# Performance work log

Measured on AMD Instinct MI355X. Metric: run time of the kernel, lower is better.

## Reference

```python
import jax, jax.numpy as jnp
import numpy as np

B, N, IN_DIM, ATT_DIM = 2, 8192, 512, 512


def setup_inputs() -> dict:
    key = jax.random.key(0)
    k1, k2, k3, k4 = jax.random.split(key, 4)
    X = jax.random.normal(k1, (B, N, IN_DIM), dtype=jnp.float32)
    adj = jax.random.uniform(k2, (B, N, N), dtype=jnp.float32)
    mask = jnp.ones((B, N), dtype=jnp.float32)
    # Learned params (torch Linear stores W as (out,in); we store (in,out) for x @ W)
    Wqk = jax.random.normal(k3, (IN_DIM, 2 * ATT_DIM), dtype=jnp.float32) / np.sqrt(IN_DIM)
    Wv = jax.random.normal(k4, (IN_DIM, IN_DIM), dtype=jnp.float32) / np.sqrt(IN_DIM)
    return {"X": X, "adj": adj, "mask": mask, "Wqk": Wqk, "Wv": Wv}


def reference(X, adj, mask, Wqk, Wv):
    # q, k: (B, N, att_dim); v: (B, N, in_dim)
    qk = X @ Wqk
    q, k = jnp.split(qk, 2, axis=-1)
    v = X @ Wv
    att_dim = q.shape[-1]
    inv_scale = 1.0 / jnp.sqrt(jnp.float32(att_dim))
    # Original math: w_i = inv_scale * sum_j adj_ij * m_i * m_j * (q_i . k_j).
    # Since the rank-1 mask factors (m_i m_j), fold m_j into k and m_i into the row
    # score, avoiding a second materialized NxN tensor:
    k_m = k * mask[:, :, None]                       # (B, N, att_dim)
    agg = jnp.einsum("bij,bjd->bid", adj, k_m)       # (B, N, att_dim)
    w = inv_scale * mask * jnp.einsum("bid,bid->bi", q, agg)  # (B, N)
    # softmax over the bag dimension (dim=1), then scale v rows
    L = jax.nn.softmax(w, axis=1)[:, :, None] * v    # (B, N, in_dim)
    return L
```

## Files before the change

kernel.cpp:

```cpp
#include <hip/hip_runtime.h>
#include <math.h>

#define BB 2
#define NN 8192
#define DD 512

static const float INV_SCALE = 0.04419417382415922f;

typedef short s16x8 __attribute__((ext_vector_type(8)));
typedef unsigned short u16x8 __attribute__((ext_vector_type(8)));
typedef float f32x4 __attribute__((ext_vector_type(4)));

#define AS1 __attribute__((address_space(1)))
#define AS3 __attribute__((address_space(3)))

__device__ __forceinline__ unsigned short bfbits(__bf16 h) {
    return __builtin_bit_cast(unsigned short, h);
}

__device__ __forceinline__ void gll16(const void* g, void* l) {
    __builtin_amdgcn_global_load_lds((const AS1 unsigned int*)g, (AS3 unsigned int*)l, 16, 0, 0);
}

__global__ __launch_bounds__(256) void convx_k(
    const float* __restrict__ X, unsigned short* __restrict__ Xhi,
    unsigned short* __restrict__ Xlo)
{
    long i = (long)blockIdx.x * 256 + threadIdx.x;
    float4 x = ((const float4*)X)[i];
    __bf16 h0 = (__bf16)x.x, h1 = (__bf16)x.y, h2 = (__bf16)x.z, h3 = (__bf16)x.w;
    ushort4 hi4 = make_ushort4(bfbits(h0), bfbits(h1), bfbits(h2), bfbits(h3));
    __bf16 l0 = (__bf16)(x.x - (float)h0), l1 = (__bf16)(x.y - (float)h1);
    __bf16 l2 = (__bf16)(x.z - (float)h2), l3 = (__bf16)(x.w - (float)h3);
    ushort4 lo4 = make_ushort4(bfbits(l0), bfbits(l1), bfbits(l2), bfbits(l3));
    ((ushort4*)Xhi)[i] = hi4;
    ((ushort4*)Xlo)[i] = lo4;
}

__global__ __launch_bounds__(256) void convw_k(
    const float* __restrict__ Wqk, const float* __restrict__ Wv,
    unsigned short* __restrict__ QTh, unsigned short* __restrict__ QTl,
    unsigned short* __restrict__ VTh, unsigned short* __restrict__ VTl)
{
    int i = blockIdx.x * 256 + threadIdx.x;
    float val; unsigned short *ph, *pl;
    if (i < 524288) {
        int n = i >> 9, k = i & 511;
        val = Wqk[k * 1024 + n]; ph = QTh + i; pl = QTl + i;
    } else {
        int o = i - 524288; int n = o >> 9, k = o & 511;
        val = Wv[k * 512 + n]; ph = VTh + o; pl = VTl + o;
    }
    __bf16 h = (__bf16)val;
    __bf16 l = (__bf16)(val - (float)h);
    *ph = bfbits(h); *pl = bfbits(l);
}

template <int EPI, int NT, bool AF32, int SPLITK, int MINW>
__global__ __launch_bounds__(256, MINW) void mfma_gemm(
    const void* __restrict__ A0, const void* __restrict__ A1,
    const unsigned short* __restrict__ B0, const unsigned short* __restrict__ B1,
    float* __restrict__ C,
    float* __restrict__ q, float* __restrict__ km_or_w,
    unsigned short* __restrict__ kmT, const float* __restrict__ mask,
    int N, int K, long sA, long sB, long sC)
{
    constexpr int BK = 32;
    constexpr int TILE_SH = 128 * BK;

    __shared__ unsigned short Asm[2 * TILE_SH];
    __shared__ unsigned short Bsm[2 * TILE_SH];

    const int t = threadIdx.x;
    const int wv = t >> 6, lane = t & 63;
    const int wm = wv >> 1, wn = wv & 1;
    const int batch = blockIdx.z / SPLITK;
    const int ksplit = blockIdx.z % SPLITK;
    const int klen = K / SPLITK;
    const int kbeg = ksplit * klen;
    const long m0 = blockIdx.x * 128;
    const int n0 = blockIdx.y * 128;

    const unsigned short* Bz0 = B0 + (long)batch * sB;
    const unsigned short* Bz1 = B1 ? B1 + (long)batch * sB : nullptr;
    const float* Af = AF32 ? (const float*)A0 + (long)batch * sA : nullptr;

    f32x4 acc[4][4];
#pragma unroll
    for (int i = 0; i < 4; ++i)
#pragma unroll
        for (int j = 0; j < 4; ++j) acc[i][j] = {0.f, 0.f, 0.f, 0.f};

    float4 rA[4];

    auto issueA = [&](int k0) {
#pragma unroll
        for (int u = 0; u < 2; ++u) {
            int row = t >> 1;
            int c8  = (t & 1) * 2 + u;
            const float* s = Af + (m0 + row) * (long)K + kbeg + k0 + c8 * 8;
            rA[2 * u]     = *(const float4*)s;
            rA[2 * u + 1] = *(const float4*)(s + 4);
        }
    };
    auto commitA = [&](int buf) {
#pragma unroll
        for (int u = 0; u < 2; ++u) {
            int row = t >> 1;
            int c8  = (t & 1) * 2 + u;
            float4 a = rA[2 * u], b = rA[2 * u + 1];
            u16x8 pk;
            pk[0] = bfbits((__bf16)a.x); pk[1] = bfbits((__bf16)a.y);
            pk[2] = bfbits((__bf16)a.z); pk[3] = bfbits((__bf16)a.w);
            pk[4] = bfbits((__bf16)b.x); pk[5] = bfbits((__bf16)b.y);
            pk[6] = bfbits((__bf16)b.z); pk[7] = bfbits((__bf16)b.w);
            *(u16x8*)(Asm + buf * TILE_SH + row * 32 + ((c8 ^ (row & 3)) << 3)) = pk;
        }
    };
    const int swzcol = ((lane & 3) ^ ((lane >> 2) & 3)) * 16;
    auto stageA16 = [&](int term, int k0, int buf) {
        const unsigned short* Ab = (term < 2) ? (const unsigned short*)A0
                                              : (const unsigned short*)A1;
#pragma unroll
        for (int u = 0; u < 2; ++u) {
            int c = wv * 2 + u;
            int row = c * 16 + (lane >> 2);
            gll16((const char*)Ab + ((m0 + row) * (long)K + kbeg + k0) * 2 + swzcol,
                  (char*)Asm + buf * (TILE_SH * 2) + c * 1024);
        }
    };
    auto stageB16 = [&](int term, int k0, int buf) {
        const unsigned short* Bb = (NT == 3 && term == 1) ? Bz1 : Bz0;
#pragma unroll
        for (int u = 0; u < 2; ++u) {
            int c = wv * 2 + u;
            int row = c * 16 + (lane >> 2);
            gll16((const char*)Bb + ((long)(n0 + row) * K + kbeg + k0) * 2 + swzcol,
                  (char*)Bsm + buf * (TILE_SH * 2) + c * 1024);
        }
    };

    if constexpr (AF32) {
        issueA(0);
        stageB16(0, 0, 0);
        commitA(0);
    } else {
        stageA16(0, 0, 0);
        stageB16(0, 0, 0);
    }
    __syncthreads();

    const int NTILES = NT * (klen / BK);
    int cur = 0, term = 0, k0 = 0;
    const int g = lane >> 4;

#pragma unroll 2
    for (int tt = 0; tt < NTILES; ++tt) {
        int k0n = k0 + BK, termn = term;
        if (k0n == klen) { k0n = 0; ++termn; }
        const bool hasNext = (tt + 1 < NTILES);

        if (hasNext) {
            if constexpr (AF32) issueA(k0n);
            else stageA16(termn, k0n, cur ^ 1);
            stageB16(termn, k0n, cur ^ 1);
        }

        s16x8 av[4], bv[4];
#pragma unroll
        for (int f = 0; f < 4; ++f) {
            int ra = wm * 64 + f * 16 + (lane & 15);
            int rb = wn * 64 + f * 16 + (lane & 15);
            av[f] = *(const s16x8*)(Asm + cur * TILE_SH + ra * BK + ((g ^ (ra & 3)) << 3));
            bv[f] = *(const s16x8*)(Bsm + cur * TILE_SH + rb * BK + ((g ^ (rb & 3)) << 3));
        }
#pragma unroll
        for (int fm = 0; fm < 4; ++fm)
#pragma unroll
            for (int fn = 0; fn < 4; ++fn)
                acc[fm][fn] = __builtin_amdgcn_mfma_f32_16x16x32_bf16(
                    av[fm], bv[fn], acc[fm][fn], 0, 0, 0);

        if (AF32 && hasNext) commitA(cur ^ 1);

        __syncthreads();
        cur ^= 1; term = termn; k0 = k0n;
    }

    const long rbase = m0 + wm * 64;
    const int cbase = n0 + wn * 64;

    if constexpr (EPI == 0) {
        float* Cz = C + (long)batch * sC;
#pragma unroll
        for (int fm = 0; fm < 4; ++fm) {
            long rb = rbase + fm * 16 + ((lane >> 4) << 2);
#pragma unroll
            for (int fn = 0; fn < 4; ++fn) {
                int c = cbase + fn * 16 + (lane & 15);
#pragma unroll
                for (int j = 0; j < 4; ++j)
                    Cz[(rb + j) * (long)N + c] = acc[fm][fn][j];
            }
        }
    } else if constexpr (EPI == 1) {
        const bool isq = (n0 < 512);
#pragma unroll
        for (int fm = 0; fm < 4; ++fm) {
            long rb = rbase + fm * 16 + ((lane >> 4) << 2);
#pragma unroll
            for (int fn = 0; fn < 4; ++fn) {
                int c = cbase + fn * 16 + (lane & 15);
                if (isq) {
#pragma unroll
                    for (int j = 0; j < 4; ++j)
                        q[(rb + j) * 512L + c] = acc[fm][fn][j];
                } else {
                    int c2 = c - 512;
                    float kv[4];
#pragma unroll
                    for (int j = 0; j < 4; ++j) {
                        kv[j] = acc[fm][fn][j] * mask[rb + j];
                        km_or_w[(rb + j) * 512L + c2] = kv[j];
                    }
                    ushort4 pk = make_ushort4(bfbits((__bf16)kv[0]), bfbits((__bf16)kv[1]),
                                              bfbits((__bf16)kv[2]), bfbits((__bf16)kv[3]));
                    long b = rb >> 13, r = rb & 8191;
                    *(ushort4*)(kmT + (b << 22) + ((long)c2 << 13) + r) = pk;
                }
            }
        }
    } else {
        const long zrow = (long)batch * NN;
#pragma unroll
        for (int fm = 0; fm < 4; ++fm) {
#pragma unroll
            for (int j = 0; j < 4; ++j) {
                long r = zrow + rbase + fm * 16 + ((lane >> 4) << 2) + j;
                const float* qr = q + r * 512L + cbase + (lane & 15);
                float s = 0.f;
#pragma unroll
                for (int fn = 0; fn < 4; ++fn)
                    s += qr[fn * 16] * acc[fm][fn][j];
                s += __shfl_xor(s, 1); s += __shfl_xor(s, 2);
                s += __shfl_xor(s, 4); s += __shfl_xor(s, 8);
                if ((lane & 15) == 0) atomicAdd(km_or_w + r, s);
            }
        }
    }
}

__global__ __launch_bounds__(256) void fixup_k(
    float* __restrict__ w, const float* __restrict__ mask)
{
    int i = blockIdx.x * 256 + threadIdx.x;
    w[i] *= INV_SCALE * mask[i];
}

__global__ __launch_bounds__(256) void wmax_k(const float* __restrict__ w,
                                              float* __restrict__ wmax)
{
    const int b = blockIdx.x;
    const float* wr = w + (long)b * NN;
    const int t = threadIdx.x;
    float m = -3.4e38f;
    for (int i = t; i < NN; i += 256) m = fmaxf(m, wr[i]);
#pragma unroll
    for (int o = 32; o > 0; o >>= 1) m = fmaxf(m, __shfl_down(m, o));
    __shared__ float red[4];
    if ((t & 63) == 0) red[t >> 6] = m;
    __syncthreads();
    if (t == 0) wmax[b] = fmaxf(fmaxf(red[0], red[1]), fmaxf(red[2], red[3]));
}

__global__ __launch_bounds__(256) void select_k(
    const float* __restrict__ w, const float* __restrict__ wmax,
    int* __restrict__ count, int* __restrict__ cand)
{
    int i = blockIdx.x * 256 + threadIdx.x;
    int b = i >> 13;
    if (w[i] >= wmax[b] - 15.f) {
        int p = atomicAdd(count, 1);
        if (p < 128) cand[p] = i;
    }
}

__global__ __launch_bounds__(256) void refine_k(
    const float* __restrict__ q, const float* __restrict__ km,
    const float* __restrict__ adj, const int* __restrict__ cand,
    const int* __restrict__ count, float* __restrict__ partial)
{
    int y = blockIdx.y;
    int cnt = *count; if (cnt > 128) cnt = 128;
    if (y >= cnt) return;
    const int row = cand[y];
    const int b = row >> 13, r = row & 8191;
    const int x = blockIdx.x;
    const int t = threadIdx.x, w = t >> 6, l = t & 63;

    const float* qr = q + (long)row * 512 + l * 8;
    const float4 q0 = *(const float4*)qr;
    const float4 q1 = *(const float4*)(qr + 4);
    const float* kmB = km + ((long)b << 13) * 512;
    const float* adjR = adj + (((long)b << 13) + r) * 8192L;

    float acc = 0.f;
    const int jbase = x * 128 + w * 32;
    for (int i = 0; i < 32; ++i) {
        int j = jbase + i;
        const float* kr = kmB + (long)j * 512 + l * 8;
        const float4 k0 = *(const float4*)kr;
        const float4 k1 = *(const float4*)(kr + 4);
        float d = q0.x * k0.x + q0.y * k0.y + q0.z * k0.z + q0.w * k0.w
                + q1.x * k1.x + q1.y * k1.y + q1.z * k1.z + q1.w * k1.w;
#pragma unroll
        for (int o = 32; o > 0; o >>= 1) d += __shfl_down(d, o);
        if (l == 0) acc += adjR[j] * d;
    }
    __shared__ float red[4];
    if (l == 0) red[w] = acc;
    __syncthreads();
    if (t == 0) partial[y * 64 + x] = red[0] + red[1] + red[2] + red[3];
}

__global__ __launch_bounds__(128) void apply_k(
    const int* __restrict__ cand, const int* __restrict__ count,
    const float* __restrict__ partial, const float* __restrict__ mask,
    float* __restrict__ w)
{
    int t = threadIdx.x;
    int cnt = *count; if (cnt > 128) cnt = 128;
    if (t < cnt) {
        float s = 0.f;
        for (int x = 0; x < 64; ++x) s += partial[t * 64 + x];
        int row = cand[t];
        w[row] = s * INV_SCALE * mask[row];
    }
}

__global__ __launch_bounds__(1024) void softmax_k(
    const float* __restrict__ w, float* __restrict__ p)
{
    const int b = blockIdx.x;
    const float* wr = w + (long)b * NN;
    float* pr = p + (long)b * NN;
    const int t = threadIdx.x;
    __shared__ float red[16];
    __shared__ float bmax, bsum;

    float m = -3.4e38f;
    for (int i = t; i < NN; i += 1024) m = fmaxf(m, wr[i]);
#pragma unroll
    for (int o = 32; o > 0; o >>= 1) m = fmaxf(m, __shfl_down(m, o));
    if ((t & 63) == 0) red[t >> 6] = m;
    __syncthreads();
    if (t == 0) {
        float mm = red[0];
        for (int i = 1; i < 16; ++i) mm = fmaxf(mm, red[i]);
        bmax = mm;
    }
    __syncthreads();
    const float M = bmax;

    float s = 0.f;
    for (int i = t; i < NN; i += 1024) s += expf(wr[i] - M);
#pragma unroll
    for (int o = 32; o > 0; o >>= 1) s += __shfl_down(s, o);
    __syncthreads();
    if ((t & 63) == 0) red[t >> 6] = s;
    __syncthreads();
    if (t == 0) {
        float ss = 0.f;
        for (int i = 0; i < 16; ++i) ss += red[i];
        bsum = ss;
    }
    __syncthreads();
    const float invS = 1.f / bsum;
    for (int i = t; i < NN; i += 1024) pr[i] = expf(wr[i] - M) * invS;
}

__global__ __launch_bounds__(256) void scale_k(
    const float* __restrict__ v, const float* __restrict__ p,
    float* __restrict__ out)
{
    const long i = (long)blockIdx.x * 256 + threadIdx.x;
    const int row = (int)(i >> 7);
    const float pv = p[row];
    float4 vv = ((const float4*)v)[i];
    vv.x *= pv; vv.y *= pv; vv.z *= pv; vv.w *= pv;
    ((float4*)out)[i] = vv;
}

extern "C" void kernel_launch(void* const* d_in, const int* in_sizes, int n_in,
                              void* d_out, int out_size, void* d_ws, size_t ws_size,
                              hipStream_t stream)
{
    const float* X    = (const float*)d_in[0];
    const float* adj  = (const float*)d_in[1];
    const float* mask = (const float*)d_in[2];
    const float* Wqk  = (const float*)d_in[3];
    const float* Wv   = (const float*)d_in[4];
    float* out = (float*)d_out;

    char* ws = (char*)d_ws;
    const long SZB = 33554432;
    float* q_buf  = (float*)(ws);
    float* km_buf = (float*)(ws + SZB);
    float* v_buf  = (float*)(ws + 2 * SZB);
    unsigned short* Xhi = (unsigned short*)(ws + 3 * SZB);
    unsigned short* Xlo = Xhi + 8388608;
    unsigned short* kmT = (unsigned short*)(ws + 4 * SZB);
    unsigned short* QTh = (unsigned short*)(ws + 4 * SZB + 16777216);
    unsigned short* QTl = QTh + 524288;
    unsigned short* VTh = QTl + 524288;
    unsigned short* VTl = VTh + 262144;
    float* w_buf = (float*)(VTl + 262144);
    float* p_buf = w_buf + 16384;
    float* wmax  = p_buf + 16384;
    float* partial = wmax + 64;
    int* count = (int*)(partial + 8192);
    int* cand  = count + 64;

    hipMemsetAsync(count, 0, 4, stream);
    hipMemsetAsync(w_buf, 0, 16384 * 4, stream);

    convx_k<<<8192, 256, 0, stream>>>(X, Xhi, Xlo);
    convw_k<<<3072, 256, 0, stream>>>(Wqk, Wv, QTh, QTl, VTh, VTl);

    mfma_gemm<1, 3, false, 1, 2><<<dim3(128, 8, 1), 256, 0, stream>>>(
        Xhi, Xlo, QTh, QTl, nullptr, q_buf, km_buf, kmT, mask,
        1024, 512, 0, 0, 0);

    mfma_gemm<0, 1, false, 1, 2><<<dim3(128, 4, 1), 256, 0, stream>>>(
        Xhi, nullptr, VTh, nullptr, v_buf, nullptr, nullptr, nullptr, nullptr,
        512, 512, 0, 0, 0);

    mfma_gemm<2, 1, true, 2, 4><<<dim3(64, 4, 4), 256, 0, stream>>>(
        adj, nullptr, kmT, nullptr, nullptr, q_buf, w_buf, nullptr, nullptr,
        512, 8192, (long)8192 * 8192, (long)512 * 8192, 0);

    fixup_k<<<64, 256, 0, stream>>>(w_buf, mask);

    wmax_k<<<BB, 256, 0, stream>>>(w_buf, wmax);
    select_k<<<64, 256, 0, stream>>>(w_buf, wmax, count, cand);
    refine_k<<<dim3(64, 128, 1), 256, 0, stream>>>(q_buf, km_buf, adj, cand, count, partial);
    apply_k<<<1, 128, 0, stream>>>(cand, count, partial, mask, w_buf);

    softmax_k<<<BB, 1024, 0, stream>>>(w_buf, p_buf);
    scale_k<<<8192, 256, 0, stream>>>(v_buf, p_buf, out);
}
```

Measured before the change: 479.1 us.

## Split adj GEMM into dedicated kernel with BK=64 and deeper register prefetch

```diff
diff --git a/kernel.cpp b/kernel.cpp
--- a/kernel.cpp
+++ b/kernel.cpp
@@ -56,14 +56,14 @@
     *ph = bfbits(h); *pl = bfbits(l);
 }
 
-template <int EPI, int NT, bool AF32, int SPLITK, int MINW>
-__global__ __launch_bounds__(256, MINW) void mfma_gemm(
-    const void* __restrict__ A0, const void* __restrict__ A1,
+template <int EPI, int NT>
+__global__ __launch_bounds__(256, 2) void mfma_gemm(
+    const unsigned short* __restrict__ A0, const unsigned short* __restrict__ A1,
     const unsigned short* __restrict__ B0, const unsigned short* __restrict__ B1,
     float* __restrict__ C,
-    float* __restrict__ q, float* __restrict__ km_or_w,
+    float* __restrict__ q, float* __restrict__ km,
     unsigned short* __restrict__ kmT, const float* __restrict__ mask,
-    int N, int K, long sA, long sB, long sC)
+    int N, int K)
 {
     constexpr int BK = 32;
     constexpr int TILE_SH = 128 * BK;
@@ -74,95 +74,53 @@
     const int t = threadIdx.x;
     const int wv = t >> 6, lane = t & 63;
     const int wm = wv >> 1, wn = wv & 1;
-    const int batch = blockIdx.z / SPLITK;
-    const int ksplit = blockIdx.z % SPLITK;
-    const int klen = K / SPLITK;
-    const int kbeg = ksplit * klen;
     const long m0 = blockIdx.x * 128;
     const int n0 = blockIdx.y * 128;
 
-    const unsigned short* Bz0 = B0 + (long)batch * sB;
-    const unsigned short* Bz1 = B1 ? B1 + (long)batch * sB : nullptr;
-    const float* Af = AF32 ? (const float*)A0 + (long)batch * sA : nullptr;
-
     f32x4 acc[4][4];
 #pragma unroll
     for (int i = 0; i < 4; ++i)
 #pragma unroll
         for (int j = 0; j < 4; ++j) acc[i][j] = {0.f, 0.f, 0.f, 0.f};
 
-    float4 rA[4];
-
-    auto issueA = [&](int k0) {
-#pragma unroll
-        for (int u = 0; u < 2; ++u) {
-            int row = t >> 1;
-            int c8  = (t & 1) * 2 + u;
-            const float* s = Af + (m0 + row) * (long)K + kbeg + k0 + c8 * 8;
-            rA[2 * u]     = *(const float4*)s;
-            rA[2 * u + 1] = *(const float4*)(s + 4);
-        }
-    };
-    auto commitA = [&](int buf) {
-#pragma unroll
-        for (int u = 0; u < 2; ++u) {
-            int row = t >> 1;
-            int c8  = (t & 1) * 2 + u;
-            float4 a = rA[2 * u], b = rA[2 * u + 1];
-            u16x8 pk;
-            pk[0] = bfbits((__bf16)a.x); pk[1] = bfbits((__bf16)a.y);
-            pk[2] = bfbits((__bf16)a.z); pk[3] = bfbits((__bf16)a.w);
-            pk[4] = bfbits((__bf16)b.x); pk[5] = bfbits((__bf16)b.y);
-            pk[6] = bfbits((__bf16)b.z); pk[7] = bfbits((__bf16)b.w);
-            *(u16x8*)(Asm + buf * TILE_SH + row * 32 + ((c8 ^ (row & 3)) << 3)) = pk;
-        }
-    };
     const int swzcol = ((lane & 3) ^ ((lane >> 2) & 3)) * 16;
     auto stageA16 = [&](int term, int k0, int buf) {
-        const unsigned short* Ab = (term < 2) ? (const unsigned short*)A0
-                                              : (const unsigned short*)A1;
+        const unsigned short* Ab = (term < 2) ? A0 : A1;
 #pragma unroll
         for (int u = 0; u < 2; ++u) {
             int c = wv * 2 + u;
             int row = c * 16 + (lane >> 2);
-            gll16((const char*)Ab + ((m0 + row) * (long)K + kbeg + k0) * 2 + swzcol,
+            gll16((const char*)Ab + ((m0 + row) * (long)K + k0) * 2 + swzcol,
                   (char*)Asm + buf * (TILE_SH * 2) + c * 1024);
         }
     };
     auto stageB16 = [&](int term, int k0, int buf) {
-        const unsigned short* Bb = (NT == 3 && term == 1) ? Bz1 : Bz0;
+        const unsigned short* Bb = (NT == 3 && term == 1) ? B1 : B0;
 #pragma unroll
         for (int u = 0; u < 2; ++u) {
             int c = wv * 2 + u;
             int row = c * 16 + (lane >> 2);
-            gll16((const char*)Bb + ((long)(n0 + row) * K + kbeg + k0) * 2 + swzcol,
+            gll16((const char*)Bb + ((long)(n0 + row) * K + k0) * 2 + swzcol,
                   (char*)Bsm + buf * (TILE_SH * 2) + c * 1024);
         }
     };
 
-    if constexpr (AF32) {
-        issueA(0);
-        stageB16(0, 0, 0);
-        commitA(0);
-    } else {
-        stageA16(0, 0, 0);
-        stageB16(0, 0, 0);
-    }
-    __syncthreads();
-
-    const int NTILES = NT * (klen / BK);
+    stageA16(0, 0, 0);
+    stageB16(0, 0, 0);
+    __syncthreads();
+
+    const int NTILES = NT * (K / BK);
     int cur = 0, term = 0, k0 = 0;
     const int g = lane >> 4;
 
 #pragma unroll 2
     for (int tt = 0; tt < NTILES; ++tt) {
         int k0n = k0 + BK, termn = term;
-        if (k0n == klen) { k0n = 0; ++termn; }
+        if (k0n == K) { k0n = 0; ++termn; }
         const bool hasNext = (tt + 1 < NTILES);
 
         if (hasNext) {
-            if constexpr (AF32) issueA(k0n);
-            else stageA16(termn, k0n, cur ^ 1);
+            stageA16(termn, k0n, cur ^ 1);
             stageB16(termn, k0n, cur ^ 1);
         }
 
@@ -181,8 +139,6 @@
                 acc[fm][fn] = __builtin_amdgcn_mfma_f32_16x16x32_bf16(
                     av[fm], bv[fn], acc[fm][fn], 0, 0, 0);
 
-        if (AF32 && hasNext) commitA(cur ^ 1);
-
         __syncthreads();
         cur ^= 1; term = termn; k0 = k0n;
     }
@@ -191,7 +147,6 @@
     const int cbase = n0 + wn * 64;
 
     if constexpr (EPI == 0) {
-        float* Cz = C + (long)batch * sC;
 #pragma unroll
         for (int fm = 0; fm < 4; ++fm) {
             long rb = rbase + fm * 16 + ((lane >> 4) << 2);
@@ -200,10 +155,10 @@
                 int c = cbase + fn * 16 + (lane & 15);
 #pragma unroll
                 for (int j = 0; j < 4; ++j)
-                    Cz[(rb + j) * (long)N + c] = acc[fm][fn][j];
+                    C[(rb + j) * (long)N + c] = acc[fm][fn][j];
             }
         }
-    } else if constexpr (EPI == 1) {
+    } else {
         const bool isq = (n0 < 512);
 #pragma unroll
         for (int fm = 0; fm < 4; ++fm) {
@@ -221,7 +176,7 @@
 #pragma unroll
                     for (int j = 0; j < 4; ++j) {
                         kv[j] = acc[fm][fn][j] * mask[rb + j];
-                        km_or_w[(rb + j) * 512L + c2] = kv[j];
+                        km[(rb + j) * 512L + c2] = kv[j];
                     }
                     ushort4 pk = make_ushort4(bfbits((__bf16)kv[0]), bfbits((__bf16)kv[1]),
                                               bfbits((__bf16)kv[2]), bfbits((__bf16)kv[3]));
@@ -230,22 +185,143 @@
                 }
             }
         }
-    } else {
-        const long zrow = (long)batch * NN;
-#pragma unroll
-        for (int fm = 0; fm < 4; ++fm) {
-#pragma unroll
-            for (int j = 0; j < 4; ++j) {
-                long r = zrow + rbase + fm * 16 + ((lane >> 4) << 2) + j;
-                const float* qr = q + r * 512L + cbase + (lane & 15);
-                float s = 0.f;
+    }
+}
+
+__global__ __launch_bounds__(256, 2) void adj_gemm(
+    const float* __restrict__ adj,
+    const unsigned short* __restrict__ kmT,
+    const float* __restrict__ q,
+    float* __restrict__ w)
+{
+    constexpr int BK = 64;
+    constexpr int TS = 128 * BK;
+    constexpr int NT = NN / BK;
+
+    __shared__ unsigned short Asm[2 * TS];
+    __shared__ unsigned short Bsm[2 * TS];
+
+    const int t = threadIdx.x;
+    const int wv = t >> 6, lane = t & 63;
+    const int wm = wv >> 1, wn = wv & 1;
+    const int z = blockIdx.z;
+    const long m0 = blockIdx.x * 128;
+    const int n0 = blockIdx.y * 128;
+
+    const float* Az = adj + (long)z * NN * NN;
+    const unsigned short* Bz = kmT + ((long)z << 22);
+
+    f32x4 acc[4][4];
+#pragma unroll
+    for (int i = 0; i < 4; ++i)
+#pragma unroll
+        for (int j = 0; j < 4; ++j) acc[i][j] = {0.f, 0.f, 0.f, 0.f};
+
+    const int bswz = ((lane & 7) ^ (lane >> 3)) << 4;
+    auto stageB = [&](int ttile, int buf) {
+        const int k0 = ttile * BK;
+#pragma unroll
+        for (int u = 0; u < 4; ++u) {
+            int c = wv * 4 + u;
+            int row = c * 8 + (lane >> 3);
+            gll16((const char*)Bz + ((long)(n0 + row) * NN + k0) * 2 + bswz,
+                  (char*)Bsm + buf * (TS * 2) + c * 1024);
+        }
+    };
+
+    const int arow = t >> 1;
+    const int asl0 = (t & 1) * 4;
+    auto issueA = [&](int ttile, float4 (&r)[8]) {
+        const float* s = Az + (m0 + arow) * (long)NN + ttile * BK + asl0 * 8;
+#pragma unroll
+        for (int u = 0; u < 4; ++u) {
+            r[2 * u]     = *(const float4*)(s + u * 8);
+            r[2 * u + 1] = *(const float4*)(s + u * 8 + 4);
+        }
+    };
+    auto commitA = [&](float4 (&r)[8], int buf) {
+#pragma unroll
+        for (int u = 0; u < 4; ++u) {
+            float4 a = r[2 * u], b = r[2 * u + 1];
+            u16x8 pk;
+            pk[0] = bfbits((__bf16)a.x); pk[1] = bfbits((__bf16)a.y);
+            pk[2] = bfbits((__bf16)a.z); pk[3] = bfbits((__bf16)a.w);
+            pk[4] = bfbits((__bf16)b.x); pk[5] = bfbits((__bf16)b.y);
+            pk[6] = bfbits((__bf16)b.z); pk[7] = bfbits((__bf16)b.w);
+            *(u16x8*)(Asm + buf * TS + arow * 64 + (((asl0 + u) ^ (arow & 7)) << 3)) = pk;
+        }
+    };
+
+    const int g = lane >> 4;
+    auto compute = [&](int buf) {
+#pragma unroll
+        for (int ks = 0; ks < 2; ++ks) {
+            s16x8 av[4], bv[4];
+#pragma unroll
+            for (int f = 0; f < 4; ++f) {
+                int ra = wm * 64 + f * 16 + (lane & 15);
+                int rb = wn * 64 + f * 16 + (lane & 15);
+                av[f] = *(const s16x8*)(Asm + buf * TS + ra * 64
+                         + (((g + ks * 4) ^ (ra & 7)) << 3));
+                bv[f] = *(const s16x8*)(Bsm + buf * TS + rb * 64
+                         + (((g + ks * 4) ^ (rb & 7)) << 3));
+            }
+#pragma unroll
+            for (int fm = 0; fm < 4; ++fm)
 #pragma unroll
                 for (int fn = 0; fn < 4; ++fn)
-                    s += qr[fn * 16] * acc[fm][fn][j];
-                s += __shfl_xor(s, 1); s += __shfl_xor(s, 2);
-                s += __shfl_xor(s, 4); s += __shfl_xor(s, 8);
-                if ((lane & 15) == 0) atomicAdd(km_or_w + r, s);
-            }
+                    acc[fm][fn] = __builtin_amdgcn_mfma_f32_16x16x32_bf16(
+                        av[fm], bv[fn], acc[fm][fn], 0, 0, 0);
+        }
+    };
+
+#define CBAR() do { \
+        asm volatile("s_waitcnt vmcnt(8) lgkmcnt(0)" ::: "memory"); \
+        __builtin_amdgcn_s_barrier(); \
+        asm volatile("" ::: "memory"); \
+    } while (0)
+
+    float4 rA0[8], rA1[8];
+
+    stageB(0, 0);
+    __builtin_amdgcn_sched_barrier(0);
+    issueA(0, rA0);
+    issueA(1, rA1);
+    commitA(rA0, 0);
+    CBAR();
+
+    for (int tt = 0; tt < NT; tt += 2) {
+        if (tt + 1 < NT) stageB(tt + 1, 1);
+        __builtin_amdgcn_sched_barrier(0);
+        if (tt + 2 < NT) issueA(tt + 2, rA0);
+        compute(0);
+        if (tt + 1 < NT) commitA(rA1, 1);
+        CBAR();
+        if (tt + 2 < NT) stageB(tt + 2, 0);
+        __builtin_amdgcn_sched_barrier(0);
+        if (tt + 3 < NT) issueA(tt + 3, rA1);
+        compute(1);
+        if (tt + 2 < NT) commitA(rA0, 0);
+        CBAR();
+    }
+#undef CBAR
+
+    const long zrow = (long)z * NN;
+    const long rbase = m0 + wm * 64;
+    const int cbase = n0 + wn * 64;
+#pragma unroll
+    for (int fm = 0; fm < 4; ++fm) {
+#pragma unroll
+        for (int j = 0; j < 4; ++j) {
+            long r = zrow + rbase + fm * 16 + ((lane >> 4) << 2) + j;
+            const float* qr = q + r * 512L + cbase + (lane & 15);
+            float s = 0.f;
+#pragma unroll
+            for (int fn = 0; fn < 4; ++fn)
+                s += qr[fn * 16] * acc[fm][fn][j];
+            s += __shfl_xor(s, 1); s += __shfl_xor(s, 2);
+            s += __shfl_xor(s, 4); s += __shfl_xor(s, 8);
+            if ((lane & 15) == 0) atomicAdd(w + r, s);
         }
     }
 }
@@ -427,17 +503,14 @@
     convx_k<<<8192, 256, 0, stream>>>(X, Xhi, Xlo);
     convw_k<<<3072, 256, 0, stream>>>(Wqk, Wv, QTh, QTl, VTh, VTl);
 
-    mfma_gemm<1, 3, false, 1, 2><<<dim3(128, 8, 1), 256, 0, stream>>>(
-        Xhi, Xlo, QTh, QTl, nullptr, q_buf, km_buf, kmT, mask,
-        1024, 512, 0, 0, 0);
-
-    mfma_gemm<0, 1, false, 1, 2><<<dim3(128, 4, 1), 256, 0, stream>>>(
+    mfma_gemm<1, 3><<<dim3(128, 8, 1), 256, 0, stream>>>(
+        Xhi, Xlo, QTh, QTl, nullptr, q_buf, km_buf, kmT, mask, 1024, 512);
+
+    mfma_gemm<0, 1><<<dim3(128, 4, 1), 256, 0, stream>>>(
         Xhi, nullptr, VTh, nullptr, v_buf, nullptr, nullptr, nullptr, nullptr,
-        512, 512, 0, 0, 0);
-
-    mfma_gemm<2, 1, true, 2, 4><<<dim3(64, 4, 4), 256, 0, stream>>>(
-        adj, nullptr, kmT, nullptr, nullptr, q_buf, w_buf, nullptr, nullptr,
-        512, 8192, (long)8192 * 8192, (long)512 * 8192, 0);
+        512, 512);
+
+    adj_gemm<<<dim3(64, 4, 2), 256, 0, stream>>>(adj, kmT, q_buf, w_buf);
 
     fixup_k<<<64, 256, 0, stream>>>(w_buf, mask);
 
```

Measured after the change: 513.5 us. 7.2% more time.
